# Kernel optimization log

Hardware: AMD Instinct MI355X
Metric: run time of the kernel (lower is better)

Reference implementation:

```python
import math
import jax, jax.numpy as jnp
import numpy as np

LAMBDA_INIT = 0.8
GN_EPS = 1e-5

B, H, S, D = 2, 16, 2048, 128  # batch, heads, seq, head_dim


def setup_inputs() -> dict:
    key = jax.random.key(0)
    ks = jax.random.split(key, 8)
    return {
        "q": jax.random.normal(ks[0], (B, H, S, 2 * D), dtype=jnp.float32),
        "k": jax.random.normal(ks[1], (B, H, S, 2 * D), dtype=jnp.float32),
        "v": jax.random.normal(ks[2], (B, H, S, D), dtype=jnp.float32),
        "lam_q1": jax.random.normal(ks[3], (D,), dtype=jnp.float32),
        "lam_q2": jax.random.normal(ks[4], (D,), dtype=jnp.float32),
        "lam_k1": jax.random.normal(ks[5], (D,), dtype=jnp.float32),
        "lam_k2": jax.random.normal(ks[6], (D,), dtype=jnp.float32),
        "gn_weight": jnp.ones((H * D,), dtype=jnp.float32),
        "gn_bias": jnp.zeros((H * D,), dtype=jnp.float32),
    }


def reference(q, k, v, lam_q1, lam_q2, lam_k1, lam_k2, gn_weight, gn_bias):
    d = q.shape[-1] // 2
    scale = 1.0 / math.sqrt(d)
    Q1, Q2 = q[..., :d], q[..., d:]
    K1, K2 = k[..., :d], k[..., d:]
    # dual score matrices [B,H,S,S]
    w1 = jax.nn.softmax(jnp.einsum('bhsd,bhtd->bhst', Q1, K1) * scale, axis=-1)
    w2 = jax.nn.softmax(jnp.einsum('bhsd,bhtd->bhst', Q2, K2) * scale, axis=-1)
    lam = jnp.exp(jnp.dot(lam_q1, lam_k1)) - jnp.exp(jnp.dot(lam_q2, lam_k2)) + LAMBDA_INIT
    weights = w1 - lam * w2
    out = jnp.einsum('bhst,bhtd->bhsd', weights, v)  # [B,H,S,D]
    # GroupNorm(num_groups=H, num_channels=H*D) applied on [B, H*D, S]:
    # channel c = h*D + dd, normalization per (batch, head) over (D, S).
    mean = out.mean(axis=(2, 3), keepdims=True)
    var = out.var(axis=(2, 3), keepdims=True)
    normed = (out - mean) * jax.lax.rsqrt(var + GN_EPS)
    gamma = gn_weight.reshape(1, out.shape[1], 1, d)
    beta = gn_bias.reshape(1, out.shape[1], 1, d)
    return (normed * gamma + beta) * (1.0 - LAMBDA_INIT)
```

## Files before the change

### kernel.cpp

```cpp
#include <hip/hip_runtime.h>
#include <cstddef>

constexpr int B = 2, H = 16, S = 2048, D = 128;
constexpr int BH = B * H;
constexpr int TWOD = 2 * D;
constexpr int QTILE = 64;
constexpr int BC = 32;
constexpr int NKT = S / BC;
constexpr float SC2 = 0.08838834764831845f * 1.4426950408889634f;
constexpr float LAM_INIT = 0.8f;
constexpr float GN_EPS = 1e-5f;

typedef __attribute__((ext_vector_type(8))) short short8;
typedef __attribute__((ext_vector_type(4))) float f32x4;

__device__ __forceinline__ unsigned short f2b(float f) {
  unsigned int u = __float_as_uint(f);
  u += 0x7fffu + ((u >> 16) & 1u);
  return (unsigned short)(u >> 16);
}

__device__ __forceinline__ void async_copy16(const void* g, void* l) {
  typedef __attribute__((address_space(1))) const void gvoid;
  typedef __attribute__((address_space(3))) void lvoid;
  __builtin_amdgcn_global_load_lds((gvoid*)g, (lvoid*)l, 16, 0, 0);
}

__global__ void convk_kernel(const float* __restrict__ src, unsigned short* __restrict__ dst,
                             const float* __restrict__ lq1, const float* __restrict__ lq2,
                             const float* __restrict__ lk1, const float* __restrict__ lk2,
                             float* __restrict__ wsf) {
  if (blockIdx.x == 0 && threadIdx.x < 64) {
    int t = threadIdx.x;
    float s1 = lq1[t] * lk1[t] + lq1[t + 64] * lk1[t + 64];
    float s2 = lq2[t] * lk2[t] + lq2[t + 64] * lk2[t + 64];
#pragma unroll
    for (int off = 32; off >= 1; off >>= 1) {
      s1 += __shfl_xor(s1, off, 64);
      s2 += __shfl_xor(s2, off, 64);
    }
    if (t == 0) wsf[0] = expf(s1) - expf(s2) + LAM_INIT;
  }
  size_t i = ((size_t)blockIdx.x * 256 + threadIdx.x) * 8;
  float4 a = *(const float4*)(src + i);
  float4 b = *(const float4*)(src + i + 4);
  unsigned short u[8];
  u[0] = f2b(a.x); u[1] = f2b(a.y); u[2] = f2b(a.z); u[3] = f2b(a.w);
  u[4] = f2b(b.x); u[5] = f2b(b.y); u[6] = f2b(b.z); u[7] = f2b(b.w);
  *(uint4*)(dst + i) = *(uint4*)u;
}

__global__ void vt_kernel(const float* __restrict__ v, unsigned short* __restrict__ vtg) {
  __shared__ float tile[64][129];
  const int bh = blockIdx.y, s0 = blockIdx.x * 64, t = threadIdx.x;
#pragma unroll
  for (int i = 0; i < 8; ++i) {
    int idx = t + i * 256;
    int row = idx >> 5, c4 = idx & 31;
    float4 f = *(const float4*)(v + ((size_t)bh * S + s0 + row) * D + c4 * 4);
    tile[row][c4 * 4 + 0] = f.x; tile[row][c4 * 4 + 1] = f.y;
    tile[row][c4 * 4 + 2] = f.z; tile[row][c4 * 4 + 3] = f.w;
  }
  __syncthreads();
#pragma unroll
  for (int i = 0; i < 4; ++i) {
    int c = t + i * 256;
    int d = c >> 3, k8 = c & 7;
    unsigned short u[8];
#pragma unroll
    for (int j = 0; j < 8; ++j) u[j] = f2b(tile[k8 * 8 + j][d]);
    *(uint4*)(vtg + ((size_t)bh * D + d) * S + s0 + k8 * 8) = *(uint4*)u;
  }
}

__global__ __launch_bounds__(256, 3)
void attn_kernel(const float* __restrict__ q, const unsigned short* __restrict__ kbf,
                 const unsigned short* __restrict__ vtg,
                 float* __restrict__ wsf, float* __restrict__ out) {
  __shared__ __attribute__((aligned(16))) unsigned char smem_raw[53248];
  __shared__ float sred[2][2];
  unsigned short (*Ks)[32][256] = (unsigned short (*)[32][256])smem_raw;
  unsigned short (*Vt)[128][40] = (unsigned short (*)[128][40])(smem_raw + 32768);
  float (*Ob)[132] = (float (*)[132])smem_raw;

  const int bh = blockIdx.x, qb = blockIdx.y;
  const int q0 = qb * QTILE;
  const int tid = threadIdx.x;
  const int wave = tid >> 6, lane = tid & 63;
  const int st = wave & 1, wq = wave >> 1;
  const int quad = lane >> 4, l16 = lane & 15;
  const float lam = wsf[0];

  short8 qf[2][4];
#pragma unroll
  for (int mt = 0; mt < 2; ++mt) {
    int qrow = q0 + wq * 32 + mt * 16 + l16;
    const float* qr = q + ((size_t)bh * S + qrow) * TWOD + st * D;
#pragma unroll
    for (int ks = 0; ks < 4; ++ks) {
      const float* p = qr + ks * 32 + quad * 8;
      float4 f0 = *(const float4*)p;
      float4 f1 = *(const float4*)(p + 4);
      short8 v8;
      v8[0] = (short)f2b(f0.x * SC2); v8[1] = (short)f2b(f0.y * SC2);
      v8[2] = (short)f2b(f0.z * SC2); v8[3] = (short)f2b(f0.w * SC2);
      v8[4] = (short)f2b(f1.x * SC2); v8[5] = (short)f2b(f1.y * SC2);
      v8[6] = (short)f2b(f1.z * SC2); v8[7] = (short)f2b(f1.w * SC2);
      qf[mt][ks] = v8;
    }
  }

  const unsigned short* kbase = kbf + (size_t)bh * S * (size_t)TWOD;
  int goff[4];
#pragma unroll
  for (int i = 0; i < 4; ++i) {
    int L = i * 256 + tid;
    int row = L >> 5, cp = L & 31;
    int g = cp ^ (row & 7);
    goff[i] = row * 256 + g * 8;
  }
  const unsigned short* vbase = vtg + (size_t)bh * D * (size_t)S;
  const int vd0 = tid >> 2, vcp = tid & 3;

  f32x4 acc[2][8];
#pragma unroll
  for (int mt = 0; mt < 2; ++mt)
#pragma unroll
    for (int n = 0; n < 8; ++n) acc[mt][n] = (f32x4){0.f, 0.f, 0.f, 0.f};
  float lacc[2] = {0.f, 0.f};

  short8 pa[2];
  {
    uint4 z4 = {0u, 0u, 0u, 0u};
    pa[0] = *(short8*)&z4; pa[1] = *(short8*)&z4;
  }
  const int stq = st * 16;
  const int srcA = ((quad * 2) & 3) * 16 + l16;
  const int srcB = ((quad * 2 + 1) & 3) * 16 + l16;
  const bool hi = quad >= 2;

  auto qk = [&](int kb, f32x4 (&sa)[2][2]) {
#pragma unroll
    for (int nt = 0; nt < 2; ++nt) {
      const int row = nt * 16 + l16;
      const int rx = row & 7;
#pragma unroll
      for (int ks = 0; ks < 4; ++ks) {
        const int pos = (stq + ks * 4 + quad) ^ rx;
        const short8 kf = *(const short8*)&Ks[kb][row][pos * 8];
        sa[0][nt] = __builtin_amdgcn_mfma_f32_16x16x32_bf16(kf, qf[0][ks], sa[0][nt], 0, 0, 0);
        sa[1][nt] = __builtin_amdgcn_mfma_f32_16x16x32_bf16(kf, qf[1][ks], sa[1][nt], 0, 0, 0);
      }
    }
  };
  auto pexp_redist = [&](f32x4 (&sa)[2][2]) {
#pragma unroll
    for (int mt = 0; mt < 2; ++mt) {
      unsigned int w[2][2];
#pragma unroll
      for (int nt = 0; nt < 2; ++nt) {
        float p0 = __builtin_amdgcn_exp2f(sa[mt][nt][0]);
        float p1 = __builtin_amdgcn_exp2f(sa[mt][nt][1]);
        float p2 = __builtin_amdgcn_exp2f(sa[mt][nt][2]);
        float p3 = __builtin_amdgcn_exp2f(sa[mt][nt][3]);
        lacc[mt] += (p0 + p1) + (p2 + p3);
        w[nt][0] = (unsigned int)f2b(p0) | ((unsigned int)f2b(p1) << 16);
        w[nt][1] = (unsigned int)f2b(p2) | ((unsigned int)f2b(p3) << 16);
      }
      unsigned int a0 = (unsigned int)__shfl((int)w[0][0], srcA, 64);
      unsigned int a1 = (unsigned int)__shfl((int)w[0][1], srcA, 64);
      unsigned int a2 = (unsigned int)__shfl((int)w[0][0], srcB, 64);
      unsigned int a3 = (unsigned int)__shfl((int)w[0][1], srcB, 64);
      unsigned int b0 = (unsigned int)__shfl((int)w[1][0], srcA, 64);
      unsigned int b1 = (unsigned int)__shfl((int)w[1][1], srcA, 64);
      unsigned int b2 = (unsigned int)__shfl((int)w[1][0], srcB, 64);
      unsigned int b3 = (unsigned int)__shfl((int)w[1][1], srcB, 64);
      uint4 pu;
      pu.x = hi ? b0 : a0;
      pu.y = hi ? b1 : a1;
      pu.z = hi ? b2 : a2;
      pu.w = hi ? b3 : a3;
      pa[mt] = *(short8*)&pu;
    }
  };
  auto pv = [&](const short8 (&vf)[8]) {
#pragma unroll
    for (int nt8 = 0; nt8 < 8; ++nt8)
#pragma unroll
      for (int mt = 0; mt < 2; ++mt)
        acc[mt][nt8] = __builtin_amdgcn_mfma_f32_16x16x32_bf16(pa[mt], vf[nt8], acc[mt][nt8], 0, 0, 0);
  };

  {
    const uint4 z = {0u, 0u, 0u, 0u};
    unsigned short* vz = &Vt[1][0][0];
    for (int i = tid; i < 640; i += 256) *(uint4*)(vz + i * 8) = z;
#pragma unroll
    for (int i = 0; i < 4; ++i)
      async_copy16(kbase + goff[i], &Ks[0][0][0] + (i * 256 + tid) * 8);
    uint4 v0 = *(const uint4*)(vbase + (size_t)vd0 * S + vcp * 8);
    uint4 v1 = *(const uint4*)(vbase + (size_t)(vd0 + 64) * S + vcp * 8);
    *(uint4*)&Vt[0][vd0][vcp * 8] = v0;
    *(uint4*)&Vt[0][vd0 + 64][vcp * 8] = v1;
  }
  __syncthreads();

  for (int t = 0; t < NKT; ++t) {
    const int kbuf = t & 1;
    const int pvbuf = kbuf ^ 1;

    short8 vf[8];
#pragma unroll
    for (int nt8 = 0; nt8 < 8; ++nt8)
      vf[nt8] = *(const short8*)&Vt[pvbuf][nt8 * 16 + l16][quad * 8];

    const bool pre = (t + 1 < NKT);
    uint4 vr0, vr1;
    if (pre) {
      const unsigned short* vp = vbase + (t + 1) * BC + vcp * 8;
      vr0 = *(const uint4*)(vp + (size_t)vd0 * S);
      vr1 = *(const uint4*)(vp + (size_t)(vd0 + 64) * S);
      const unsigned short* kp = kbase + (size_t)(t + 1) * BC * TWOD;
      unsigned short* ldsb = &Ks[pvbuf][0][0];
#pragma unroll
      for (int i = 0; i < 4; ++i)
        async_copy16(kp + goff[i], ldsb + (i * 256 + tid) * 8);
    }

    f32x4 sa[2][2];
#pragma unroll
    for (int mt = 0; mt < 2; ++mt)
#pragma unroll
      for (int nt = 0; nt < 2; ++nt) sa[mt][nt] = (f32x4){0.f, 0.f, 0.f, 0.f};
    qk(kbuf, sa);
    pv(vf);
    pexp_redist(sa);

    __syncthreads();
    if (pre) {
      *(uint4*)&Vt[pvbuf][vd0][vcp * 8] = vr0;
      *(uint4*)&Vt[pvbuf][vd0 + 64][vcp * 8] = vr1;
    }
  }

  {
    short8 vf[8];
#pragma unroll
    for (int nt8 = 0; nt8 < 8; ++nt8)
      vf[nt8] = *(const short8*)&Vt[1][nt8 * 16 + l16][quad * 8];
    pv(vf);
  }

#pragma unroll
  for (int mt = 0; mt < 2; ++mt) {
    float v = lacc[mt];
    v += __shfl_xor(v, 16, 64);
    v += __shfl_xor(v, 32, 64);
    lacc[mt] = v;
  }

  const int obase = wq * 32;
  if (st == 1) {
#pragma unroll
    for (int mt = 0; mt < 2; ++mt) {
      float i2[4];
#pragma unroll
      for (int r = 0; r < 4; ++r) i2[r] = lam / __shfl(lacc[mt], quad * 4 + r, 64);
#pragma unroll
      for (int nt8 = 0; nt8 < 8; ++nt8)
#pragma unroll
        for (int r = 0; r < 4; ++r)
          Ob[obase + mt * 16 + quad * 4 + r][nt8 * 16 + l16] = acc[mt][nt8][r] * i2[r];
    }
  }
  __syncthreads();
  if (st == 0) {
    float sum = 0.f, ssq = 0.f;
#pragma unroll
    for (int mt = 0; mt < 2; ++mt) {
      float i1[4];
#pragma unroll
      for (int r = 0; r < 4; ++r) i1[r] = 1.f / __shfl(lacc[mt], quad * 4 + r, 64);
#pragma unroll
      for (int nt8 = 0; nt8 < 8; ++nt8)
#pragma unroll
        for (int r = 0; r < 4; ++r) {
          float o = acc[mt][nt8][r] * i1[r]
                  - Ob[obase + mt * 16 + quad * 4 + r][nt8 * 16 + l16];
          int row = q0 + obase + mt * 16 + quad * 4 + r;
          out[((size_t)bh * S + row) * D + nt8 * 16 + l16] = o;
          sum += o; ssq += o * o;
        }
    }
#pragma unroll
    for (int off = 32; off >= 1; off >>= 1) {
      sum += __shfl_xor(sum, off, 64);
      ssq += __shfl_xor(ssq, off, 64);
    }
    if (lane == 0) { sred[wq][0] = sum; sred[wq][1] = ssq; }
  }
  __syncthreads();
  if (tid == 0) {
    float s0 = sred[0][0] + sred[1][0];
    float s1 = sred[0][1] + sred[1][1];
    int idx = bh * 32 + qb;
    wsf[64 + idx * 2] = s0;
    wsf[64 + idx * 2 + 1] = s1;
  }
}

__global__ void gn_kernel(float* __restrict__ out, const float* __restrict__ gw,
                          const float* __restrict__ gb, const float* __restrict__ wsf) {
  const int bh = blockIdx.x, part = blockIdx.y;
  const int h = bh & (H - 1);
  float sum = 0.f, ssq = 0.f;
  for (int j = 0; j < 32; ++j) {
    sum += wsf[64 + (bh * 32 + j) * 2];
    ssq += wsf[64 + (bh * 32 + j) * 2 + 1];
  }
  const float invn = 1.f / (float)(S * D);
  const float mean = sum * invn;
  const float var = ssq * invn - mean * mean;
  const float rstd = rsqrtf(var + GN_EPS);
  const float outscale = 1.f - LAM_INIT;
  const float4* g4 = (const float4*)(gw + h * D);
  const float4* b4 = (const float4*)(gb + h * D);
  float4* o4 = (float4*)(out + (size_t)bh * S * D);
  const int chunks_per = (S * D / 4) / 8;
  const int c0 = part * chunks_per;
  for (int c = c0 + threadIdx.x; c < c0 + chunks_per; c += 256) {
    float4 vv = o4[c];
    int d4 = c & 31;
    float4 g = g4[d4], bb = b4[d4];
    vv.x = ((vv.x - mean) * rstd * g.x + bb.x) * outscale;
    vv.y = ((vv.y - mean) * rstd * g.y + bb.y) * outscale;
    vv.z = ((vv.z - mean) * rstd * g.z + bb.z) * outscale;
    vv.w = ((vv.w - mean) * rstd * g.w + bb.w) * outscale;
    o4[c] = vv;
  }
}

extern "C" void kernel_launch(void* const* d_in, const int* in_sizes, int n_in,
                              void* d_out, int out_size, void* d_ws, size_t ws_size,
                              hipStream_t stream) {
  (void)in_sizes; (void)n_in; (void)out_size; (void)ws_size;
  const float* q   = (const float*)d_in[0];
  const float* k   = (const float*)d_in[1];
  const float* v   = (const float*)d_in[2];
  const float* lq1 = (const float*)d_in[3];
  const float* lq2 = (const float*)d_in[4];
  const float* lk1 = (const float*)d_in[5];
  const float* lk2 = (const float*)d_in[6];
  const float* gw  = (const float*)d_in[7];
  const float* gb  = (const float*)d_in[8];
  float* out = (float*)d_out;
  float* wsf = (float*)d_ws;
  unsigned short* vtg = (unsigned short*)((char*)d_ws + 16384);
  unsigned short* kbf = (unsigned short*)((char*)d_ws + 16384 + (size_t)BH * D * S * 2);

  convk_kernel<<<dim3(BH * S * TWOD / 2048), dim3(256), 0, stream>>>(k, kbf, lq1, lq2, lk1, lk2, wsf);
  vt_kernel<<<dim3(S / 64, BH), dim3(256), 0, stream>>>(v, vtg);
  attn_kernel<<<dim3(BH, S / QTILE), dim3(256), 0, stream>>>(q, kbf, vtg, wsf, out);
  gn_kernel<<<dim3(BH, 8), dim3(256), 0, stream>>>(out, gw, gb, wsf);
}
```

Measured before the change: 397.2 us.

## Double key tile size and read V fragments directly from global memory

Raises the key block from 32 to 64 rows, doubling the K shared-memory double buffer and the per-iteration QK and PV work, which halves the number of loop iterations and barriers. The V shared-memory staging buffer is removed: each wave now loads its V^T MFMA operands straight from global (L2-cached) memory. At t=0 the PV step multiplies zero probabilities against tile 0 as a dummy. Larger LDS use and more registers lower launch bounds occupancy from 3 to 2 blocks per CU, and uncoalesced-ish direct global V loads may add latency.

```diff
diff --git a/kernel.cpp b/kernel.cpp
--- a/kernel.cpp
+++ b/kernel.cpp
@@ -5,7 +5,7 @@
 constexpr int BH = B * H;
 constexpr int TWOD = 2 * D;
 constexpr int QTILE = 64;
-constexpr int BC = 32;
+constexpr int BC = 64;
 constexpr int NKT = S / BC;
 constexpr float SC2 = 0.08838834764831845f * 1.4426950408889634f;
 constexpr float LAM_INIT = 0.8f;
@@ -73,14 +73,13 @@
   }
 }
 
-__global__ __launch_bounds__(256, 3)
+__global__ __launch_bounds__(256, 2)
 void attn_kernel(const float* __restrict__ q, const unsigned short* __restrict__ kbf,
                  const unsigned short* __restrict__ vtg,
                  float* __restrict__ wsf, float* __restrict__ out) {
-  __shared__ __attribute__((aligned(16))) unsigned char smem_raw[53248];
+  __shared__ __attribute__((aligned(16))) unsigned char smem_raw[65536];
   __shared__ float sred[2][2];
-  unsigned short (*Ks)[32][256] = (unsigned short (*)[32][256])smem_raw;
-  unsigned short (*Vt)[128][40] = (unsigned short (*)[128][40])(smem_raw + 32768);
+  unsigned short (*Ks)[64][256] = (unsigned short (*)[64][256])smem_raw;
   float (*Ob)[132] = (float (*)[132])smem_raw;
 
   const int bh = blockIdx.x, qb = blockIdx.y;
@@ -111,16 +110,15 @@
   }
 
   const unsigned short* kbase = kbf + (size_t)bh * S * (size_t)TWOD;
-  int goff[4];
-#pragma unroll
-  for (int i = 0; i < 4; ++i) {
+  int goff[8];
+#pragma unroll
+  for (int i = 0; i < 8; ++i) {
     int L = i * 256 + tid;
     int row = L >> 5, cp = L & 31;
     int g = cp ^ (row & 7);
     goff[i] = row * 256 + g * 8;
   }
   const unsigned short* vbase = vtg + (size_t)bh * D * (size_t)S;
-  const int vd0 = tid >> 2, vcp = tid & 3;
 
   f32x4 acc[2][8];
 #pragma unroll
@@ -129,21 +127,22 @@
     for (int n = 0; n < 8; ++n) acc[mt][n] = (f32x4){0.f, 0.f, 0.f, 0.f};
   float lacc[2] = {0.f, 0.f};
 
-  short8 pa[2];
+  short8 pa[2][2];
   {
     uint4 z4 = {0u, 0u, 0u, 0u};
-    pa[0] = *(short8*)&z4; pa[1] = *(short8*)&z4;
+    pa[0][0] = *(short8*)&z4; pa[0][1] = *(short8*)&z4;
+    pa[1][0] = *(short8*)&z4; pa[1][1] = *(short8*)&z4;
   }
   const int stq = st * 16;
   const int srcA = ((quad * 2) & 3) * 16 + l16;
   const int srcB = ((quad * 2 + 1) & 3) * 16 + l16;
   const bool hi = quad >= 2;
-
-  auto qk = [&](int kb, f32x4 (&sa)[2][2]) {
-#pragma unroll
-    for (int nt = 0; nt < 2; ++nt) {
+  const int rx = l16 & 7;
+
+  auto qk = [&](int kb, f32x4 (&sa)[2][4]) {
+#pragma unroll
+    for (int nt = 0; nt < 4; ++nt) {
       const int row = nt * 16 + l16;
-      const int rx = row & 7;
 #pragma unroll
       for (int ks = 0; ks < 4; ++ks) {
         const int pos = (stq + ks * 4 + quad) ^ rx;
@@ -153,12 +152,18 @@
       }
     }
   };
-  auto pexp_redist = [&](f32x4 (&sa)[2][2]) {
+  auto loadv = [&](int vtile, int kk, short8 (&vf)[8]) {
+    const unsigned short* vp = vbase + vtile * BC + kk * 32 + quad * 8;
+#pragma unroll
+    for (int nt8 = 0; nt8 < 8; ++nt8)
+      vf[nt8] = *(const short8*)(vp + (size_t)(nt8 * 16 + l16) * S);
+  };
+  auto pexp_redist = [&](f32x4 (&sa)[2][4]) {
 #pragma unroll
     for (int mt = 0; mt < 2; ++mt) {
-      unsigned int w[2][2];
-#pragma unroll
-      for (int nt = 0; nt < 2; ++nt) {
+      unsigned int w[4][2];
+#pragma unroll
+      for (int nt = 0; nt < 4; ++nt) {
         float p0 = __builtin_amdgcn_exp2f(sa[mt][nt][0]);
         float p1 = __builtin_amdgcn_exp2f(sa[mt][nt][1]);
         float p2 = __builtin_amdgcn_exp2f(sa[mt][nt][2]);
@@ -167,88 +172,76 @@
         w[nt][0] = (unsigned int)f2b(p0) | ((unsigned int)f2b(p1) << 16);
         w[nt][1] = (unsigned int)f2b(p2) | ((unsigned int)f2b(p3) << 16);
       }
-      unsigned int a0 = (unsigned int)__shfl((int)w[0][0], srcA, 64);
-      unsigned int a1 = (unsigned int)__shfl((int)w[0][1], srcA, 64);
-      unsigned int a2 = (unsigned int)__shfl((int)w[0][0], srcB, 64);
-      unsigned int a3 = (unsigned int)__shfl((int)w[0][1], srcB, 64);
-      unsigned int b0 = (unsigned int)__shfl((int)w[1][0], srcA, 64);
-      unsigned int b1 = (unsigned int)__shfl((int)w[1][1], srcA, 64);
-      unsigned int b2 = (unsigned int)__shfl((int)w[1][0], srcB, 64);
-      unsigned int b3 = (unsigned int)__shfl((int)w[1][1], srcB, 64);
-      uint4 pu;
-      pu.x = hi ? b0 : a0;
-      pu.y = hi ? b1 : a1;
-      pu.z = hi ? b2 : a2;
-      pu.w = hi ? b3 : a3;
-      pa[mt] = *(short8*)&pu;
+#pragma unroll
+      for (int kk = 0; kk < 2; ++kk) {
+        unsigned int a0 = (unsigned int)__shfl((int)w[2 * kk][0], srcA, 64);
+        unsigned int a1 = (unsigned int)__shfl((int)w[2 * kk][1], srcA, 64);
+        unsigned int a2 = (unsigned int)__shfl((int)w[2 * kk][0], srcB, 64);
+        unsigned int a3 = (unsigned int)__shfl((int)w[2 * kk][1], srcB, 64);
+        unsigned int b0 = (unsigned int)__shfl((int)w[2 * kk + 1][0], srcA, 64);
+        unsigned int b1 = (unsigned int)__shfl((int)w[2 * kk + 1][1], srcA, 64);
+        unsigned int b2 = (unsigned int)__shfl((int)w[2 * kk + 1][0], srcB, 64);
+        unsigned int b3 = (unsigned int)__shfl((int)w[2 * kk + 1][1], srcB, 64);
+        uint4 pu;
+        pu.x = hi ? b0 : a0;
+        pu.y = hi ? b1 : a1;
+        pu.z = hi ? b2 : a2;
+        pu.w = hi ? b3 : a3;
+        pa[kk][mt] = *(short8*)&pu;
+      }
     }
   };
-  auto pv = [&](const short8 (&vf)[8]) {
+  auto pv = [&](int kk, const short8 (&vf)[8]) {
 #pragma unroll
     for (int nt8 = 0; nt8 < 8; ++nt8)
 #pragma unroll
       for (int mt = 0; mt < 2; ++mt)
-        acc[mt][nt8] = __builtin_amdgcn_mfma_f32_16x16x32_bf16(pa[mt], vf[nt8], acc[mt][nt8], 0, 0, 0);
+        acc[mt][nt8] = __builtin_amdgcn_mfma_f32_16x16x32_bf16(pa[kk][mt], vf[nt8], acc[mt][nt8], 0, 0, 0);
   };
 
+#pragma unroll
+  for (int i = 0; i < 8; ++i)
+    async_copy16(kbase + goff[i], (unsigned short*)smem_raw + (i * 256 + tid) * 8);
+  __syncthreads();
+
+  for (int t = 0; t < NKT; ++t) {
+    const int kb = t & 1;
+    const int vtile = (t > 0) ? (t - 1) : 0;
+
+    short8 vf0[8];
+    loadv(vtile, 0, vf0);
+
+    const bool pre = (t + 1 < NKT);
+    if (pre) {
+      const unsigned short* kp = kbase + (size_t)(t + 1) * BC * TWOD;
+      unsigned short* ldsb = (unsigned short*)smem_raw + (size_t)(kb ^ 1) * 16384;
+#pragma unroll
+      for (int i = 0; i < 8; ++i)
+        async_copy16(kp + goff[i], ldsb + (i * 256 + tid) * 8);
+    }
+
+    f32x4 sa[2][4];
+#pragma unroll
+    for (int mt = 0; mt < 2; ++mt)
+#pragma unroll
+      for (int nt = 0; nt < 4; ++nt) sa[mt][nt] = (f32x4){0.f, 0.f, 0.f, 0.f};
+    qk(kb, sa);
+
+    short8 vf1[8];
+    loadv(vtile, 1, vf1);
+    pv(0, vf0);
+    pv(1, vf1);
+    pexp_redist(sa);
+
+    __syncthreads();
+  }
+
   {
-    const uint4 z = {0u, 0u, 0u, 0u};
-    unsigned short* vz = &Vt[1][0][0];
-    for (int i = tid; i < 640; i += 256) *(uint4*)(vz + i * 8) = z;
-#pragma unroll
-    for (int i = 0; i < 4; ++i)
-      async_copy16(kbase + goff[i], &Ks[0][0][0] + (i * 256 + tid) * 8);
-    uint4 v0 = *(const uint4*)(vbase + (size_t)vd0 * S + vcp * 8);
-    uint4 v1 = *(const uint4*)(vbase + (size_t)(vd0 + 64) * S + vcp * 8);
-    *(uint4*)&Vt[0][vd0][vcp * 8] = v0;
-    *(uint4*)&Vt[0][vd0 + 64][vcp * 8] = v1;
-  }
-  __syncthreads();
-
-  for (int t = 0; t < NKT; ++t) {
-    const int kbuf = t & 1;
-    const int pvbuf = kbuf ^ 1;
-
-    short8 vf[8];
-#pragma unroll
-    for (int nt8 = 0; nt8 < 8; ++nt8)
-      vf[nt8] = *(const short8*)&Vt[pvbuf][nt8 * 16 + l16][quad * 8];
-
-    const bool pre = (t + 1 < NKT);
-    uint4 vr0, vr1;
-    if (pre) {
-      const unsigned short* vp = vbase + (t + 1) * BC + vcp * 8;
-      vr0 = *(const uint4*)(vp + (size_t)vd0 * S);
-      vr1 = *(const uint4*)(vp + (size_t)(vd0 + 64) * S);
-      const unsigned short* kp = kbase + (size_t)(t + 1) * BC * TWOD;
-      unsigned short* ldsb = &Ks[pvbuf][0][0];
-#pragma unroll
-      for (int i = 0; i < 4; ++i)
-        async_copy16(kp + goff[i], ldsb + (i * 256 + tid) * 8);
-    }
-
-    f32x4 sa[2][2];
-#pragma unroll
-    for (int mt = 0; mt < 2; ++mt)
-#pragma unroll
-      for (int nt = 0; nt < 2; ++nt) sa[mt][nt] = (f32x4){0.f, 0.f, 0.f, 0.f};
-    qk(kbuf, sa);
-    pv(vf);
-    pexp_redist(sa);
-
-    __syncthreads();
-    if (pre) {
-      *(uint4*)&Vt[pvbuf][vd0][vcp * 8] = vr0;
-      *(uint4*)&Vt[pvbuf][vd0 + 64][vcp * 8] = vr1;
-    }
-  }
-
-  {
-    short8 vf[8];
-#pragma unroll
-    for (int nt8 = 0; nt8 < 8; ++nt8)
-      vf[nt8] = *(const short8*)&Vt[1][nt8 * 16 + l16][quad * 8];
-    pv(vf);
+    short8 vf0[8], vf1[8];
+    loadv(NKT - 1, 0, vf0);
+    loadv(NKT - 1, 1, vf1);
+    pv(0, vf0);
+    pv(1, vf1);
   }
 
 #pragma unroll
```

Result: slower. 487.3 us (+22.7%).

## Merge prep kernels and deepen K prefetch with finer-grained waitcnt barriers

Applied to the files above, without the earlier changes.

The K-to-bf16 conversion and the V transpose kernels are merged into a single launch, removing one kernel launch and its tail. In the attention loop, the K tile prefetch is issued two iterations ahead, after the barrier, so the async global-to-LDS copy overlaps more compute. The full __syncthreads is replaced with explicit s_waitcnt plus s_barrier so V register loads stay in flight across the barrier. MFMA sections are given raised wave priority with s_setprio. The hand-written waitcnt counts must match the outstanding loads, or the kernel risks subtle races.

```diff
diff --git a/kernel.cpp b/kernel.cpp
--- a/kernel.cpp
+++ b/kernel.cpp
@@ -26,50 +26,52 @@
   __builtin_amdgcn_global_load_lds((gvoid*)g, (lvoid*)l, 16, 0, 0);
 }
 
-__global__ void convk_kernel(const float* __restrict__ src, unsigned short* __restrict__ dst,
-                             const float* __restrict__ lq1, const float* __restrict__ lq2,
-                             const float* __restrict__ lk1, const float* __restrict__ lk2,
-                             float* __restrict__ wsf) {
-  if (blockIdx.x == 0 && threadIdx.x < 64) {
-    int t = threadIdx.x;
-    float s1 = lq1[t] * lk1[t] + lq1[t + 64] * lk1[t + 64];
-    float s2 = lq2[t] * lk2[t] + lq2[t + 64] * lk2[t + 64];
-#pragma unroll
-    for (int off = 32; off >= 1; off >>= 1) {
-      s1 += __shfl_xor(s1, off, 64);
-      s2 += __shfl_xor(s2, off, 64);
-    }
-    if (t == 0) wsf[0] = expf(s1) - expf(s2) + LAM_INIT;
-  }
-  size_t i = ((size_t)blockIdx.x * 256 + threadIdx.x) * 8;
-  float4 a = *(const float4*)(src + i);
-  float4 b = *(const float4*)(src + i + 4);
-  unsigned short u[8];
-  u[0] = f2b(a.x); u[1] = f2b(a.y); u[2] = f2b(a.z); u[3] = f2b(a.w);
-  u[4] = f2b(b.x); u[5] = f2b(b.y); u[6] = f2b(b.z); u[7] = f2b(b.w);
-  *(uint4*)(dst + i) = *(uint4*)u;
-}
-
-__global__ void vt_kernel(const float* __restrict__ v, unsigned short* __restrict__ vtg) {
+__global__ void prep_kernel(const float* __restrict__ ksrc, unsigned short* __restrict__ kdst,
+                            const float* __restrict__ v, unsigned short* __restrict__ vtg,
+                            const float* __restrict__ lq1, const float* __restrict__ lq2,
+                            const float* __restrict__ lk1, const float* __restrict__ lk2,
+                            float* __restrict__ wsf) {
   __shared__ float tile[64][129];
-  const int bh = blockIdx.y, s0 = blockIdx.x * 64, t = threadIdx.x;
-#pragma unroll
-  for (int i = 0; i < 8; ++i) {
-    int idx = t + i * 256;
-    int row = idx >> 5, c4 = idx & 31;
-    float4 f = *(const float4*)(v + ((size_t)bh * S + s0 + row) * D + c4 * 4);
-    tile[row][c4 * 4 + 0] = f.x; tile[row][c4 * 4 + 1] = f.y;
-    tile[row][c4 * 4 + 2] = f.z; tile[row][c4 * 4 + 3] = f.w;
-  }
-  __syncthreads();
-#pragma unroll
-  for (int i = 0; i < 4; ++i) {
-    int c = t + i * 256;
-    int d = c >> 3, k8 = c & 7;
+  const int t = threadIdx.x;
+  if (blockIdx.x < 8192) {
+    if (blockIdx.x == 0 && t < 64) {
+      float s1 = lq1[t] * lk1[t] + lq1[t + 64] * lk1[t + 64];
+      float s2 = lq2[t] * lk2[t] + lq2[t + 64] * lk2[t + 64];
+#pragma unroll
+      for (int off = 32; off >= 1; off >>= 1) {
+        s1 += __shfl_xor(s1, off, 64);
+        s2 += __shfl_xor(s2, off, 64);
+      }
+      if (t == 0) wsf[0] = expf(s1) - expf(s2) + LAM_INIT;
+    }
+    size_t i = ((size_t)blockIdx.x * 256 + t) * 8;
+    float4 a = *(const float4*)(ksrc + i);
+    float4 b = *(const float4*)(ksrc + i + 4);
     unsigned short u[8];
-#pragma unroll
-    for (int j = 0; j < 8; ++j) u[j] = f2b(tile[k8 * 8 + j][d]);
-    *(uint4*)(vtg + ((size_t)bh * D + d) * S + s0 + k8 * 8) = *(uint4*)u;
+    u[0] = f2b(a.x); u[1] = f2b(a.y); u[2] = f2b(a.z); u[3] = f2b(a.w);
+    u[4] = f2b(b.x); u[5] = f2b(b.y); u[6] = f2b(b.z); u[7] = f2b(b.w);
+    *(uint4*)(kdst + i) = *(uint4*)u;
+  } else {
+    const int bid = blockIdx.x - 8192;
+    const int bh = bid >> 5, s0 = (bid & 31) * 64;
+#pragma unroll
+    for (int i = 0; i < 8; ++i) {
+      int idx = t + i * 256;
+      int row = idx >> 5, c4 = idx & 31;
+      float4 f = *(const float4*)(v + ((size_t)bh * S + s0 + row) * D + c4 * 4);
+      tile[row][c4 * 4 + 0] = f.x; tile[row][c4 * 4 + 1] = f.y;
+      tile[row][c4 * 4 + 2] = f.z; tile[row][c4 * 4 + 3] = f.w;
+    }
+    __syncthreads();
+#pragma unroll
+    for (int i = 0; i < 4; ++i) {
+      int c = t + i * 256;
+      int d = c >> 3, k8 = c & 7;
+      unsigned short u[8];
+#pragma unroll
+      for (int j = 0; j < 8; ++j) u[j] = f2b(tile[k8 * 8 + j][d]);
+      *(uint4*)(vtg + ((size_t)bh * D + d) * S + s0 + k8 * 8) = *(uint4*)u;
+    }
   }
 }
 
@@ -200,55 +202,75 @@
       async_copy16(kbase + goff[i], &Ks[0][0][0] + (i * 256 + tid) * 8);
     uint4 v0 = *(const uint4*)(vbase + (size_t)vd0 * S + vcp * 8);
     uint4 v1 = *(const uint4*)(vbase + (size_t)(vd0 + 64) * S + vcp * 8);
+    asm volatile("s_waitcnt vmcnt(0)\n\ts_waitcnt lgkmcnt(0)" ::: "memory");
+    __builtin_amdgcn_s_barrier();
     *(uint4*)&Vt[0][vd0][vcp * 8] = v0;
     *(uint4*)&Vt[0][vd0 + 64][vcp * 8] = v1;
-  }
-  __syncthreads();
-
-  for (int t = 0; t < NKT; ++t) {
-    const int kbuf = t & 1;
-    const int pvbuf = kbuf ^ 1;
+    const unsigned short* kp = kbase + (size_t)BC * TWOD;
+#pragma unroll
+    for (int i = 0; i < 4; ++i)
+      async_copy16(kp + goff[i], &Ks[1][0][0] + (i * 256 + tid) * 8);
+  }
+
+  for (int t = 0; t < NKT - 1; ++t) {
+    const int kb = t & 1;
+    const int pvb = kb ^ 1;
 
     short8 vf[8];
 #pragma unroll
     for (int nt8 = 0; nt8 < 8; ++nt8)
-      vf[nt8] = *(const short8*)&Vt[pvbuf][nt8 * 16 + l16][quad * 8];
-
-    const bool pre = (t + 1 < NKT);
-    uint4 vr0, vr1;
-    if (pre) {
-      const unsigned short* vp = vbase + (t + 1) * BC + vcp * 8;
-      vr0 = *(const uint4*)(vp + (size_t)vd0 * S);
-      vr1 = *(const uint4*)(vp + (size_t)(vd0 + 64) * S);
-      const unsigned short* kp = kbase + (size_t)(t + 1) * BC * TWOD;
-      unsigned short* ldsb = &Ks[pvbuf][0][0];
+      vf[nt8] = *(const short8*)&Vt[pvb][nt8 * 16 + l16][quad * 8];
+
+    const unsigned short* vp = vbase + (t + 1) * BC + vcp * 8;
+    uint4 vr0 = *(const uint4*)(vp + (size_t)vd0 * S);
+    uint4 vr1 = *(const uint4*)(vp + (size_t)(vd0 + 64) * S);
+
+    f32x4 sa[2][2];
+#pragma unroll
+    for (int mt = 0; mt < 2; ++mt)
+#pragma unroll
+      for (int nt = 0; nt < 2; ++nt) sa[mt][nt] = (f32x4){0.f, 0.f, 0.f, 0.f};
+    __builtin_amdgcn_s_setprio(1);
+    qk(kb, sa);
+    pv(vf);
+    __builtin_amdgcn_s_setprio(0);
+    pexp_redist(sa);
+
+    asm volatile("s_waitcnt lgkmcnt(0)\n\ts_waitcnt vmcnt(2)" ::: "memory");
+    __builtin_amdgcn_s_barrier();
+    asm volatile("s_waitcnt vmcnt(0)" ::: "memory");
+    *(uint4*)&Vt[pvb][vd0][vcp * 8] = vr0;
+    *(uint4*)&Vt[pvb][vd0 + 64][vcp * 8] = vr1;
+    if (t < NKT - 2) {
+      const unsigned short* kp = kbase + (size_t)(t + 2) * BC * TWOD;
+      unsigned short* ldsb = &Ks[kb][0][0];
 #pragma unroll
       for (int i = 0; i < 4; ++i)
         async_copy16(kp + goff[i], ldsb + (i * 256 + tid) * 8);
     }
-
+  }
+
+  {
+    const int kb = (NKT - 1) & 1, pvb = kb ^ 1;
+    short8 vf[8];
+#pragma unroll
+    for (int nt8 = 0; nt8 < 8; ++nt8)
+      vf[nt8] = *(const short8*)&Vt[pvb][nt8 * 16 + l16][quad * 8];
     f32x4 sa[2][2];
 #pragma unroll
     for (int mt = 0; mt < 2; ++mt)
 #pragma unroll
       for (int nt = 0; nt < 2; ++nt) sa[mt][nt] = (f32x4){0.f, 0.f, 0.f, 0.f};
-    qk(kbuf, sa);
+    qk(kb, sa);
     pv(vf);
     pexp_redist(sa);
-
-    __syncthreads();
-    if (pre) {
-      *(uint4*)&Vt[pvbuf][vd0][vcp * 8] = vr0;
-      *(uint4*)&Vt[pvbuf][vd0 + 64][vcp * 8] = vr1;
-    }
-  }
-
-  {
-    short8 vf[8];
+    asm volatile("s_waitcnt lgkmcnt(0)" ::: "memory");
+    __builtin_amdgcn_s_barrier();
+    short8 vf2[8];
 #pragma unroll
     for (int nt8 = 0; nt8 < 8; ++nt8)
-      vf[nt8] = *(const short8*)&Vt[1][nt8 * 16 + l16][quad * 8];
-    pv(vf);
+      vf2[nt8] = *(const short8*)&Vt[kb][nt8 * 16 + l16][quad * 8];
+    pv(vf2);
   }
 
 #pragma unroll
@@ -260,6 +282,7 @@
   }
 
   const int obase = wq * 32;
+  __syncthreads();
   if (st == 1) {
 #pragma unroll
     for (int mt = 0; mt < 2; ++mt) {
@@ -358,8 +381,7 @@
   unsigned short* vtg = (unsigned short*)((char*)d_ws + 16384);
   unsigned short* kbf = (unsigned short*)((char*)d_ws + 16384 + (size_t)BH * D * S * 2);
 
-  convk_kernel<<<dim3(BH * S * TWOD / 2048), dim3(256), 0, stream>>>(k, kbf, lq1, lq2, lk1, lk2, wsf);
-  vt_kernel<<<dim3(S / 64, BH), dim3(256), 0, stream>>>(v, vtg);
+  prep_kernel<<<dim3(8192 + BH * 32), dim3(256), 0, stream>>>(k, kbf, v, vtg, lq1, lq2, lk1, lk2, wsf);
   attn_kernel<<<dim3(BH, S / QTILE), dim3(256), 0, stream>>>(q, kbf, vtg, wsf, out);
   gn_kernel<<<dim3(BH, 8), dim3(256), 0, stream>>>(out, gw, gb, wsf);
 }
```

Measured after the change: 605.7 us. 1.52x slower.
